# Kernel tuning notes

Hardware: AMD Instinct MI355X
Metric: run time of the kernel (lower is better)

The kernel has to match this reference:

```python
import jax, jax.numpy as jnp
import numpy as np

N_NODES = 100000
N_EDGES = 1600000
IN_CH = 24
OUT_CH = 128


def _linear_params(key, fan_in, fan_out):
    k1, k2 = jax.random.split(key)
    s = 1.0 / np.sqrt(fan_in)
    w = jax.random.uniform(k1, (fan_in, fan_out), jnp.float32, -s, s)
    b = jax.random.uniform(k2, (fan_out,), jnp.float32, -s, s)
    return w, b


def setup_inputs() -> dict:
    key = jax.random.key(0)
    ks = jax.random.split(key, 10)
    x = jax.random.normal(ks[0], (N_NODES, IN_CH), jnp.float32)
    edge_index = jax.random.randint(ks[1], (2, N_EDGES), 0, N_NODES, jnp.int64)
    w1a, b1a = _linear_params(ks[2], 2 * IN_CH, OUT_CH)
    w1b, b1b = _linear_params(ks[3], OUT_CH, OUT_CH)
    w2a, b2a = _linear_params(ks[4], 2 * OUT_CH, OUT_CH)
    w2b, b2b = _linear_params(ks[5], OUT_CH, OUT_CH)
    w3a, b3a = _linear_params(ks[6], 2 * OUT_CH, OUT_CH)
    w3b, b3b = _linear_params(ks[7], OUT_CH, OUT_CH)
    fw, fb = _linear_params(ks[8], 16, 1)
    return dict(x=x, edge_index=edge_index,
                w1a=w1a, b1a=b1a, w1b=w1b, b1b=b1b,
                w2a=w2a, b2a=b2a, w2b=w2b, b2b=b2b,
                w3a=w3a, b3a=b3a, w3b=w3b, b3b=b3b,
                fw=fw, fb=fb)


def _edge_conv(x, src, dst, wa, ba, wb, bb):
    # gather endpoints: x_i = target, x_j = source (PyG convention)
    x_i = x[dst]
    x_j = x[src]
    tmp = jnp.concatenate([x_i, x_j - x_i], axis=1)        # [E, 2*C]
    msg = jax.nn.relu(tmp @ wa + ba) @ wb + bb             # [E, out]
    agg = jax.ops.segment_max(msg, dst, num_segments=N_NODES)
    # PyG max-aggr yields 0 for nodes with no incoming edges
    return jnp.where(jnp.isneginf(agg), 0.0, agg)


def reference(x, edge_index, w1a, b1a, w1b, b1b, w2a, b2a, w2b, b2b,
              w3a, b3a, w3b, b3b, fw, fb):
    src = edge_index[0]
    dst = edge_index[1]
    x2 = jax.nn.relu(_edge_conv(x, src, dst, w1a, b1a, w1b, b1b))
    x4 = jax.nn.relu(_edge_conv(x2, src, dst, w2a, b2a, w2b, b2b))
    x6 = jax.nn.relu(_edge_conv(x4, src, dst, w3a, b3a, w3b, b3b))
    x7 = jnp.concatenate([x2, x4, x6], axis=1)             # [N, 3*OUT_CH]
    # MaxPool1d(kernel=IN_CH, stride=IN_CH) over last dim: 384 -> 16
    x8 = x7.reshape(N_NODES, 3 * OUT_CH // IN_CH, IN_CH).max(axis=-1)
    return x8 @ fw + fb                                     # [N, 1]
```

## Files before the change

### kernel.cpp

```cpp
#include <hip/hip_runtime.h>
#include <stdint.h>

#define NN 100000
#define NE 1600000
#define MAXD 64

using short8 = __attribute__((ext_vector_type(8))) short;
using f32x4  = __attribute__((ext_vector_type(4))) float;
using u32x4  = __attribute__((ext_vector_type(4))) unsigned int;
typedef unsigned short ushort_t;

__device__ __forceinline__ ushort_t f2bf(float f){
  union { float f; uint32_t u; } v; v.f = f;
  uint32_t u = v.u;
  uint32_t r = (u + 0x7fffu + ((u >> 16) & 1u)) >> 16;
  return (ushort_t)r;
}
__device__ __forceinline__ float bf2f(ushort_t h){
  union { uint32_t u; float f; } v; v.u = ((uint32_t)h) << 16;
  return v.f;
}

__global__ void k_detect(const unsigned* ei, int* flag){
  __shared__ int any;
  if(threadIdx.x == 0) any = 0;
  __syncthreads();
  unsigned w = ei[2*threadIdx.x + 1];
  if(w) atomicOr(&any, 1);
  __syncthreads();
  if(threadIdx.x == 0) *flag = (any == 0) ? 1 : 0;
}

__global__ void k_build(const int* ei, const int* flag, int* cursor, int* list){
  int e = blockIdx.x * blockDim.x + threadIdx.x;
  if(e >= NE) return;
  bool i64 = (*flag != 0);
  int src, dst;
  if(i64){
    const long long* p = (const long long*)ei;
    src = (int)p[e]; dst = (int)p[NE + e];
  } else {
    src = ei[e]; dst = ei[NE + e];
  }
  if((unsigned)src >= NN || (unsigned)dst >= NN) return;
  int pos = atomicAdd(&cursor[dst], 1);
  if(pos < MAXD) list[dst*MAXD + pos] = src;
}

__global__ void k_wcatfrag(const float* wa, ushort_t* dst, int C, int KT){
  int idx = blockIdx.x*blockDim.x + threadIdx.x;
  int total = 16*KT*64*8;
  if(idx >= total) return;
  int j = idx & 7, lane = (idx>>3)&63;
  int rest = idx >> 9;
  int kt = rest % KT, nt = rest / KT;
  int k = kt*32 + ((lane>>4)<<3) + j;
  int n = nt*16 + (lane & 15);
  float v = 0.f;
  if(k < C) v = (n < 128) ? (wa[k*128+n] - wa[(C+k)*128+n]) : wa[(C+k)*128 + (n-128)];
  dst[idx] = f2bf(v);
}

__global__ void k_wbfrag(const float* wb, ushort_t* dst){
  int idx = blockIdx.x*blockDim.x + threadIdx.x;
  if(idx >= 8*4*64*8) return;
  int j = idx & 7, lane = (idx>>3)&63;
  int kt = (idx>>9)&3, nt = idx>>11;
  int k = kt*32 + ((lane>>4)<<3) + j;
  int n = nt*16 + (lane & 15);
  dst[idx] = f2bf(wb[k*128 + n]);
}

template<int KT, int ROWLEN, bool SPLIT>
__global__ __launch_bounds__(256)
void k_gemm(const void* xin_, const ushort_t* __restrict__ wfrag,
            const float* __restrict__ bias, float* __restrict__ Atab,
            ushort_t* __restrict__ Btab)
{
  constexpr int K  = KT*32;
  constexpr int RB = K*2 + 16;
  __shared__ ushort_t shHi[64*RB/2];
  __shared__ ushort_t shLo[SPLIT ? 64*RB/2 : 2];

  const int t = threadIdx.x;
  const int wave = t >> 6, lane = t & 63;
  const int l15 = lane & 15, lg = lane >> 4;

  short8 bf[4][KT];
  #pragma unroll
  for(int ntl=0; ntl<4; ntl++)
    #pragma unroll
    for(int kt=0; kt<KT; kt++){
      int nt = wave*4 + ntl;
      bf[ntl][kt] = *(const short8*)&wfrag[((nt*KT + kt)*64 + lane)*8];
    }
  float bv[4] = {0.f,0.f,0.f,0.f};
  if(wave < 2){
    #pragma unroll
    for(int ntl=0; ntl<4; ntl++) bv[ntl] = bias[wave*64 + ntl*16 + l15];
  }

  const int row0 = blockIdx.x * 64;

  constexpr int GROUPS = 64*(K/8);
  #pragma unroll
  for(int it=0; it<GROUPS/256; it++){
    int gi  = t + it*256;
    int row = gi / (K/8), kg = gi % (K/8);
    int gr  = row0 + row;
    int off = (row*RB + kg*16) >> 1;
    if constexpr (SPLIT){
      const float* xin = (const float*)xin_;
      short8 hi8, lo8;
      #pragma unroll
      for(int j=0;j<8;j++){
        int k = kg*8 + j;
        float v = (gr < NN && k < ROWLEN) ? xin[(size_t)gr*ROWLEN + k] : 0.f;
        ushort_t h = f2bf(v);
        hi8[j] = (short)h;
        lo8[j] = (short)f2bf(v - bf2f(h));
      }
      *(short8*)&shHi[off] = hi8;
      *(short8*)&shLo[off] = lo8;
    } else {
      const ushort_t* xb = (const ushort_t*)xin_;
      short8 h8 = {0,0,0,0,0,0,0,0};
      if(gr < NN) h8 = *(const short8*)&xb[(size_t)gr*ROWLEN + kg*8];
      *(short8*)&shHi[off] = h8;
    }
  }
  __syncthreads();

  #pragma unroll
  for(int mc=0; mc<4; mc++){
    f32x4 acc[4];
    #pragma unroll
    for(int ntl=0; ntl<4; ntl++) acc[ntl] = (f32x4){0.f,0.f,0.f,0.f};
    #pragma unroll
    for(int kt=0; kt<KT; kt++){
      int off = ((mc*16 + l15)*RB + kt*64 + lg*16) >> 1;
      short8 ah = *(const short8*)&shHi[off];
      #pragma unroll
      for(int ntl=0; ntl<4; ntl++)
        acc[ntl] = __builtin_amdgcn_mfma_f32_16x16x32_bf16(ah, bf[ntl][kt], acc[ntl], 0,0,0);
      if constexpr (SPLIT){
        short8 al = *(const short8*)&shLo[off];
        #pragma unroll
        for(int ntl=0; ntl<4; ntl++)
          acc[ntl] = __builtin_amdgcn_mfma_f32_16x16x32_bf16(al, bf[ntl][kt], acc[ntl], 0,0,0);
      }
    }
    #pragma unroll
    for(int ntl=0; ntl<4; ntl++){
      #pragma unroll
      for(int q=0; q<4; q++){
        int gr = row0 + mc*16 + lg*4 + q;
        if(gr < NN){
          if(wave < 2){
            int ch = wave*64 + ntl*16 + l15;
            Atab[(size_t)gr*128 + ch] = acc[ntl][q] + bv[ntl];
          } else {
            int ch = (wave-2)*64 + ntl*16 + l15;
            Btab[(size_t)gr*128 + ch] = f2bf(acc[ntl][q]);
          }
        }
      }
    }
  }
}

template<bool F32OUT>
__global__ __launch_bounds__(256)
void k_edge(const float* __restrict__ Atab, const ushort_t* __restrict__ Btab,
            const ushort_t* __restrict__ wbfrag, const float* __restrict__ bias2,
            const int* __restrict__ deg, const int* __restrict__ list,
            float* __restrict__ outF, ushort_t* __restrict__ outB)
{
  __shared__ ushort_t shH[2][16*272/2];

  const int t = threadIdx.x;
  const int wave = t >> 6, lane = t & 63;
  const int l15 = lane & 15, lg = lane >> 4;
  const int eg  = t >> 4;
  const int cg  = t & 15;

  short8 wf[2][4];
  #pragma unroll
  for(int ntl=0; ntl<2; ntl++)
    #pragma unroll
    for(int kt=0; kt<4; kt++){
      int nt = wave*2 + ntl;
      wf[ntl][kt] = *(const short8*)&wbfrag[((nt*4 + kt)*64 + lane)*8];
    }
  float bbv[2];
  #pragma unroll
  for(int ntl=0; ntl<2; ntl++) bbv[ntl] = bias2[wave*32 + ntl*16 + l15];

  int buf = 0;
  for(int n = blockIdx.x; n < NN; n += gridDim.x){
    int d = deg[n]; if(d > MAXD) d = MAXD;
    if(d == 0){
      if(lane < 16){
        #pragma unroll
        for(int ntl=0; ntl<2; ntl++){
          int ch = wave*32 + ntl*16 + lane;
          if(F32OUT) outF[(size_t)n*128 + ch] = 0.f;
          else       outB[(size_t)n*128 + ch] = 0;
        }
      }
      continue;
    }
    const int* lst = &list[(size_t)n*MAXD];
    const float4* ap = (const float4*)&Atab[(size_t)n*128 + cg*8];
    float4 a0 = ap[0], a1 = ap[1];
    float af[8] = {a0.x,a0.y,a0.z,a0.w,a1.x,a1.y,a1.z,a1.w};

    f32x4 mac0 = (f32x4){-3.0e38f,-3.0e38f,-3.0e38f,-3.0e38f};
    f32x4 mac1 = mac0;

    int nch = (d + 15) >> 4;
    int ei0 = (eg < d) ? eg : d - 1;
    short8 b8 = *(const short8*)&Btab[(size_t)lst[ei0]*128 + cg*8];

    for(int c = 0; c < nch; c++){
      union { short8 s; uint32_t u[4]; } bb; bb.s = b8;
      u32x4 pkv;
      #pragma unroll
      for(int p=0; p<4; p++){
        uint32_t w = bb.u[p];
        float flo = __uint_as_float(w << 16);
        float fhi = __uint_as_float(w & 0xffff0000u);
        float hlo = fmaxf(af[2*p]   + flo, 0.f);
        float hhi = fmaxf(af[2*p+1] + fhi, 0.f);
        uint32_t pw;
        asm("v_cvt_pk_bf16_f32 %0, %1, %2" : "=v"(pw) : "v"(hlo), "v"(hhi));
        pkv[p] = pw;
      }
      *(u32x4*)&shH[buf][(eg*272 + cg*16) >> 1] = pkv;

      if(c + 1 < nch){
        int e2 = (c+1)*16 + eg; if(e2 >= d) e2 = d - 1;
        b8 = *(const short8*)&Btab[(size_t)lst[e2]*128 + cg*8];
      }

      __syncthreads();

      f32x4 acc0 = (f32x4){0.f,0.f,0.f,0.f};
      f32x4 acc1 = (f32x4){0.f,0.f,0.f,0.f};
      #pragma unroll
      for(int kt=0; kt<4; kt++){
        short8 a = *(const short8*)&shH[buf][(l15*272 + kt*64 + lg*16) >> 1];
        acc0 = __builtin_amdgcn_mfma_f32_16x16x32_bf16(a, wf[0][kt], acc0, 0,0,0);
        acc1 = __builtin_amdgcn_mfma_f32_16x16x32_bf16(a, wf[1][kt], acc1, 0,0,0);
      }
      #pragma unroll
      for(int q=0; q<4; q++){
        mac0[q] = fmaxf(mac0[q], acc0[q]);
        mac1[q] = fmaxf(mac1[q], acc1[q]);
      }
      buf ^= 1;
    }

    float mm0 = fmaxf(fmaxf(mac0[0],mac0[1]), fmaxf(mac0[2],mac0[3]));
    mm0 = fmaxf(mm0, __shfl_xor(mm0, 16, 64));
    mm0 = fmaxf(mm0, __shfl_xor(mm0, 32, 64));
    float mm1 = fmaxf(fmaxf(mac1[0],mac1[1]), fmaxf(mac1[2],mac1[3]));
    mm1 = fmaxf(mm1, __shfl_xor(mm1, 16, 64));
    mm1 = fmaxf(mm1, __shfl_xor(mm1, 32, 64));

    if(lane < 16){
      float v0 = fmaxf(mm0 + bbv[0], 0.f);
      float v1 = fmaxf(mm1 + bbv[1], 0.f);
      int ch = wave*32 + lane;
      if(F32OUT){
        outF[(size_t)n*128 + ch]      = v0;
        outF[(size_t)n*128 + ch + 16] = v1;
      } else {
        outB[(size_t)n*128 + ch]      = f2bf(v0);
        outB[(size_t)n*128 + ch + 16] = f2bf(v1);
      }
    }
  }
}

template<bool F32IN>
__global__ __launch_bounds__(256)
void k_final(const void* x2_, const void* x4_, const void* x6_,
             const float* __restrict__ fw, const float* __restrict__ fb,
             float* __restrict__ out)
{
  __shared__ float arr[4][384];
  int wave = threadIdx.x >> 6, lane = threadIdx.x & 63;
  int n = blockIdx.x*4 + wave;
  if(n < NN){
    const void* xs[3] = {x2_, x4_, x6_};
    #pragma unroll
    for(int tt=0; tt<3; tt++){
      float a, b;
      if(F32IN){
        const float* p = (const float*)xs[tt] + (size_t)n*128 + lane*2;
        a = p[0]; b = p[1];
      } else {
        const ushort_t* p = (const ushort_t*)xs[tt] + (size_t)n*128 + lane*2;
        a = bf2f(p[0]); b = bf2f(p[1]);
      }
      arr[wave][tt*128 + lane*2]     = a;
      arr[wave][tt*128 + lane*2 + 1] = b;
    }
  }
  __syncthreads();
  if(n < NN && lane < 16){
    float m = -3.0e38f;
    #pragma unroll
    for(int j=0;j<24;j++) m = fmaxf(m, arr[wave][lane*24 + j]);
    float p = m * fw[lane];
    #pragma unroll
    for(int off=1; off<16; off<<=1) p += __shfl_xor(p, off, 64);
    if(lane == 0) out[n] = p + fb[0];
  }
}

extern "C" void kernel_launch(void* const* d_in, const int* in_sizes, int n_in,
                              void* d_out, int out_size, void* d_ws, size_t ws_size,
                              hipStream_t stream)
{
  const float* x   = (const float*)d_in[0];
  const void*  ei  = d_in[1];
  const float* w1a = (const float*)d_in[2];
  const float* b1a = (const float*)d_in[3];
  const float* w1b = (const float*)d_in[4];
  const float* b1b = (const float*)d_in[5];
  const float* w2a = (const float*)d_in[6];
  const float* b2a = (const float*)d_in[7];
  const float* w2b = (const float*)d_in[8];
  const float* b2b = (const float*)d_in[9];
  const float* w3a = (const float*)d_in[10];
  const float* b3a = (const float*)d_in[11];
  const float* w3b = (const float*)d_in[12];
  const float* b3b = (const float*)d_in[13];
  const float* fw  = (const float*)d_in[14];
  const float* fb  = (const float*)d_in[15];

  char* ws = (char*)d_ws;
  size_t off = 0;
  auto alloc = [&](size_t bytes) -> void* {
    void* p = ws + off;
    off = (off + bytes + 255) & ~(size_t)255;
    return p;
  };
  int*      flag   = (int*)alloc(4);
  int*      cursor = (int*)alloc((size_t)NN*4);
  int*      list   = (int*)alloc((size_t)NN*MAXD*4);
  float*    Atab   = (float*)alloc((size_t)NN*128*4);
  ushort_t* Btab   = (ushort_t*)alloc((size_t)NN*128*2);
  ushort_t* wf1    = (ushort_t*)alloc(16*1*64*8*2);
  ushort_t* wf2    = (ushort_t*)alloc(16*4*64*8*2);
  ushort_t* wf3    = (ushort_t*)alloc(16*4*64*8*2);
  ushort_t* wbf1   = (ushort_t*)alloc(8*4*64*8*2);
  ushort_t* wbf2   = (ushort_t*)alloc(8*4*64*8*2);
  ushort_t* wbf3   = (ushort_t*)alloc(8*4*64*8*2);

  size_t fixed = off;
  bool planA = (ws_size >= fixed + 3*(size_t)NN*128*4 + 1024);
  void *x2, *x4, *x6;
  size_t xbytes = planA ? (size_t)NN*128*4 : (size_t)NN*128*2;
  x2 = alloc(xbytes); x4 = alloc(xbytes); x6 = alloc(xbytes);

  hipMemsetAsync(cursor, 0, (size_t)NN*4, stream);
  k_detect<<<1, 128, 0, stream>>>((const unsigned*)ei, flag);
  k_build<<<(NE + 255)/256, 256, 0, stream>>>((const int*)ei, flag, cursor, list);

  k_wcatfrag<<<(16*1*64*8 + 255)/256, 256, 0, stream>>>(w1a, wf1, 24, 1);
  k_wcatfrag<<<(16*4*64*8 + 255)/256, 256, 0, stream>>>(w2a, wf2, 128, 4);
  k_wcatfrag<<<(16*4*64*8 + 255)/256, 256, 0, stream>>>(w3a, wf3, 128, 4);
  k_wbfrag<<<64, 256, 0, stream>>>(w1b, wbf1);
  k_wbfrag<<<64, 256, 0, stream>>>(w2b, wbf2);
  k_wbfrag<<<64, 256, 0, stream>>>(w3b, wbf3);

  const int GT = (NN + 63)/64;
  const int EG = 4096;

  k_gemm<1,24,true><<<GT, 256, 0, stream>>>(x, wf1, b1a, Atab, Btab);
  if(planA){
    k_edge<true><<<EG, 256, 0, stream>>>(Atab, Btab, wbf1, b1b, cursor, list, (float*)x2, nullptr);
    k_gemm<4,128,true><<<GT, 256, 0, stream>>>(x2, wf2, b2a, Atab, Btab);
    k_edge<true><<<EG, 256, 0, stream>>>(Atab, Btab, wbf2, b2b, cursor, list, (float*)x4, nullptr);
    k_gemm<4,128,true><<<GT, 256, 0, stream>>>(x4, wf3, b3a, Atab, Btab);
    k_edge<true><<<EG, 256, 0, stream>>>(Atab, Btab, wbf3, b3b, cursor, list, (float*)x6, nullptr);
    k_final<true><<<(NN + 3)/4, 256, 0, stream>>>(x2, x4, x6, fw, fb, (float*)d_out);
  } else {
    k_edge<false><<<EG, 256, 0, stream>>>(Atab, Btab, wbf1, b1b, cursor, list, nullptr, (ushort_t*)x2);
    k_gemm<4,128,false><<<GT, 256, 0, stream>>>(x2, wf2, b2a, Atab, Btab);
    k_edge<false><<<EG, 256, 0, stream>>>(Atab, Btab, wbf2, b2b, cursor, list, nullptr, (ushort_t*)x4);
    k_gemm<4,128,false><<<GT, 256, 0, stream>>>(x4, wf3, b3a, Atab, Btab);
    k_edge<false><<<EG, 256, 0, stream>>>(Atab, Btab, wbf3, b3b, cursor, list, nullptr, (ushort_t*)x6);
    k_final<false><<<(NN + 3)/4, 256, 0, stream>>>(x2, x4, x6, fw, fb, (float*)d_out);
  }
}
```

Before: 842.0 us.

## Assign one node per wave in edge kernel, dropping block-wide barriers

The edge kernel now processes one destination node per wavefront instead of one per 256-thread block. Each wave gathers its own 16 neighbor rows, writes them to a private swizzled LDS tile, and computes all 8 output column tiles itself with MFMA. This removes the per-chunk __syncthreads and lets the four waves in a block run independently. In exchange, the second-layer weight fragments are reloaded from global memory on every chunk instead of being held in registers, and register pressure rises, with launch bounds set to request 4 blocks per SM.

```diff
diff --git a/kernel.cpp b/kernel.cpp
--- a/kernel.cpp
+++ b/kernel.cpp
@@ -170,114 +170,118 @@
 }
 
 template<bool F32OUT>
-__global__ __launch_bounds__(256)
+__global__ __launch_bounds__(256, 4)
 void k_edge(const float* __restrict__ Atab, const ushort_t* __restrict__ Btab,
             const ushort_t* __restrict__ wbfrag, const float* __restrict__ bias2,
             const int* __restrict__ deg, const int* __restrict__ list,
             float* __restrict__ outF, ushort_t* __restrict__ outB)
 {
-  __shared__ ushort_t shH[2][16*272/2];
+  __shared__ ushort_t sh[4][16*136];
 
   const int t = threadIdx.x;
   const int wave = t >> 6, lane = t & 63;
-  const int l15 = lane & 15, lg = lane >> 4;
-  const int eg  = t >> 4;
-  const int cg  = t & 15;
-
-  short8 wf[2][4];
+  const int r  = lane & 15;
+  const int qq = lane >> 4;
+  const int sw = ((qq ^ (r & 3)) * 8);
+  const int rbase = r * 136;
+  ushort_t* msh = sh[wave];
+
+  float bb[8];
   #pragma unroll
-  for(int ntl=0; ntl<2; ntl++)
-    #pragma unroll
-    for(int kt=0; kt<4; kt++){
-      int nt = wave*2 + ntl;
-      wf[ntl][kt] = *(const short8*)&wbfrag[((nt*4 + kt)*64 + lane)*8];
-    }
-  float bbv[2];
-  #pragma unroll
-  for(int ntl=0; ntl<2; ntl++) bbv[ntl] = bias2[wave*32 + ntl*16 + l15];
-
-  int buf = 0;
-  for(int n = blockIdx.x; n < NN; n += gridDim.x){
+  for(int nt=0; nt<8; nt++) bb[nt] = bias2[nt*16 + r];
+
+  for(int n = blockIdx.x*4 + wave; n < NN; n += gridDim.x*4){
     int d = deg[n]; if(d > MAXD) d = MAXD;
     if(d == 0){
       if(lane < 16){
         #pragma unroll
-        for(int ntl=0; ntl<2; ntl++){
-          int ch = wave*32 + ntl*16 + lane;
-          if(F32OUT) outF[(size_t)n*128 + ch] = 0.f;
-          else       outB[(size_t)n*128 + ch] = 0;
+        for(int nt=0; nt<8; nt++){
+          if(F32OUT) outF[(size_t)n*128 + nt*16 + lane] = 0.f;
+          else       outB[(size_t)n*128 + nt*16 + lane] = 0;
         }
       }
       continue;
     }
     const int* lst = &list[(size_t)n*MAXD];
-    const float4* ap = (const float4*)&Atab[(size_t)n*128 + cg*8];
-    float4 a0 = ap[0], a1 = ap[1];
-    float af[8] = {a0.x,a0.y,a0.z,a0.w,a1.x,a1.y,a1.z,a1.w};
-
-    f32x4 mac0 = (f32x4){-3.0e38f,-3.0e38f,-3.0e38f,-3.0e38f};
-    f32x4 mac1 = mac0;
+
+    float a[4][8];
+    #pragma unroll
+    for(int i=0;i<4;i++){
+      f32x4 lo = *(const f32x4*)&Atab[(size_t)n*128 + i*32 + qq*8];
+      f32x4 hi = *(const f32x4*)&Atab[(size_t)n*128 + i*32 + qq*8 + 4];
+      #pragma unroll
+      for(int j=0;j<4;j++){ a[i][j] = lo[j]; a[i][4+j] = hi[j]; }
+    }
+
+    f32x4 mac[8];
+    #pragma unroll
+    for(int nt=0;nt<8;nt++)
+      mac[nt] = (f32x4){-3.0e38f,-3.0e38f,-3.0e38f,-3.0e38f};
 
     int nch = (d + 15) >> 4;
-    int ei0 = (eg < d) ? eg : d - 1;
-    short8 b8 = *(const short8*)&Btab[(size_t)lst[ei0]*128 + cg*8];
-
-    for(int c = 0; c < nch; c++){
-      union { short8 s; uint32_t u[4]; } bb; bb.s = b8;
-      u32x4 pkv;
-      #pragma unroll
-      for(int p=0; p<4; p++){
-        uint32_t w = bb.u[p];
-        float flo = __uint_as_float(w << 16);
-        float fhi = __uint_as_float(w & 0xffff0000u);
-        float hlo = fmaxf(af[2*p]   + flo, 0.f);
-        float hhi = fmaxf(af[2*p+1] + fhi, 0.f);
-        uint32_t pw;
-        asm("v_cvt_pk_bf16_f32 %0, %1, %2" : "=v"(pw) : "v"(hlo), "v"(hhi));
-        pkv[p] = pw;
-      }
-      *(u32x4*)&shH[buf][(eg*272 + cg*16) >> 1] = pkv;
+    int e0 = r; if(e0 >= d) e0 = d - 1;
+    int s = lst[e0];
+    short8 bw[4];
+    #pragma unroll
+    for(int i=0;i<4;i++)
+      bw[i] = *(const short8*)&Btab[(size_t)s*128 + i*32 + qq*8];
+
+    for(int c = 0; c < nch; ++c){
+      u32x4 pk[4];
+      #pragma unroll
+      for(int i=0;i<4;i++){
+        union { short8 s8; uint32_t u[4]; } ub; ub.s8 = bw[i];
+        #pragma unroll
+        for(int w2=0; w2<4; ++w2){
+          uint32_t u = ub.u[w2];
+          float flo = __uint_as_float(u << 16);
+          float fhi = __uint_as_float(u & 0xffff0000u);
+          float hlo = fmaxf(a[i][2*w2]   + flo, 0.f);
+          float hhi = fmaxf(a[i][2*w2+1] + fhi, 0.f);
+          uint32_t pw;
+          asm("v_cvt_pk_bf16_f32 %0, %1, %2" : "=v"(pw) : "v"(hlo), "v"(hhi));
+          pk[i][w2] = pw;
+        }
+      }
+      asm volatile("s_waitcnt lgkmcnt(0)" ::: "memory");
+      #pragma unroll
+      for(int i=0;i<4;i++)
+        *(u32x4*)&msh[rbase + i*32 + sw] = pk[i];
 
       if(c + 1 < nch){
-        int e2 = (c+1)*16 + eg; if(e2 >= d) e2 = d - 1;
-        b8 = *(const short8*)&Btab[(size_t)lst[e2]*128 + cg*8];
-      }
-
-      __syncthreads();
-
-      f32x4 acc0 = (f32x4){0.f,0.f,0.f,0.f};
-      f32x4 acc1 = (f32x4){0.f,0.f,0.f,0.f};
-      #pragma unroll
-      for(int kt=0; kt<4; kt++){
-        short8 a = *(const short8*)&shH[buf][(l15*272 + kt*64 + lg*16) >> 1];
-        acc0 = __builtin_amdgcn_mfma_f32_16x16x32_bf16(a, wf[0][kt], acc0, 0,0,0);
-        acc1 = __builtin_amdgcn_mfma_f32_16x16x32_bf16(a, wf[1][kt], acc1, 0,0,0);
-      }
-      #pragma unroll
-      for(int q=0; q<4; q++){
-        mac0[q] = fmaxf(mac0[q], acc0[q]);
-        mac1[q] = fmaxf(mac1[q], acc1[q]);
-      }
-      buf ^= 1;
-    }
-
-    float mm0 = fmaxf(fmaxf(mac0[0],mac0[1]), fmaxf(mac0[2],mac0[3]));
-    mm0 = fmaxf(mm0, __shfl_xor(mm0, 16, 64));
-    mm0 = fmaxf(mm0, __shfl_xor(mm0, 32, 64));
-    float mm1 = fmaxf(fmaxf(mac1[0],mac1[1]), fmaxf(mac1[2],mac1[3]));
-    mm1 = fmaxf(mm1, __shfl_xor(mm1, 16, 64));
-    mm1 = fmaxf(mm1, __shfl_xor(mm1, 32, 64));
-
-    if(lane < 16){
-      float v0 = fmaxf(mm0 + bbv[0], 0.f);
-      float v1 = fmaxf(mm1 + bbv[1], 0.f);
-      int ch = wave*32 + lane;
-      if(F32OUT){
-        outF[(size_t)n*128 + ch]      = v0;
-        outF[(size_t)n*128 + ch + 16] = v1;
-      } else {
-        outB[(size_t)n*128 + ch]      = f2bf(v0);
-        outB[(size_t)n*128 + ch + 16] = f2bf(v1);
+        int e2 = (c+1)*16 + r; if(e2 >= d) e2 = d - 1;
+        s = lst[e2];
+        #pragma unroll
+        for(int i=0;i<4;i++)
+          bw[i] = *(const short8*)&Btab[(size_t)s*128 + i*32 + qq*8];
+      }
+
+      short8 af[4];
+      #pragma unroll
+      for(int kt=0; kt<4; ++kt)
+        af[kt] = *(const short8*)&msh[rbase + kt*32 + sw];
+      #pragma unroll
+      for(int nt=0; nt<8; ++nt){
+        f32x4 acc = (f32x4){0.f,0.f,0.f,0.f};
+        #pragma unroll
+        for(int kt=0; kt<4; ++kt){
+          short8 wfr = *(const short8*)&wbfrag[((nt*4 + kt)*64 + lane)*8];
+          acc = __builtin_amdgcn_mfma_f32_16x16x32_bf16(af[kt], wfr, acc, 0,0,0);
+        }
+        #pragma unroll
+        for(int q=0;q<4;q++) mac[nt][q] = fmaxf(mac[nt][q], acc[q]);
+      }
+    }
+
+    #pragma unroll
+    for(int nt=0; nt<8; ++nt){
+      float m = fmaxf(fmaxf(mac[nt][0],mac[nt][1]), fmaxf(mac[nt][2],mac[nt][3]));
+      m = fmaxf(m, __shfl_xor(m, 16, 64));
+      m = fmaxf(m, __shfl_xor(m, 32, 64));
+      float v = fmaxf(m + bb[nt], 0.f);
+      if(lane < 16){
+        if(F32OUT) outF[(size_t)n*128 + nt*16 + lane] = v;
+        else       outB[(size_t)n*128 + nt*16 + lane] = f2bf(v);
       }
     }
   }
```

Measured after the change: 2.544 ms. 202% more time.

## Process two destination nodes per block iteration in edge kernel

Applied to the files above, without the earlier changes.

The edge-message kernel now handles a pair of destination nodes per loop iteration. Each node has its own LDS staging buffers, running max accumulators and gather prefetches, and both share one barrier per chunk. This is meant to halve the number of __syncthreads per node and keep more gather loads and MFMA work in flight to hide memory latency. In exchange it raises register pressure and adds per-node branches, and when the two nodes differ in degree the extra chunks only partly fill the work.

```diff
diff --git a/kernel.cpp b/kernel.cpp
--- a/kernel.cpp
+++ b/kernel.cpp
@@ -176,7 +176,7 @@
             const int* __restrict__ deg, const int* __restrict__ list,
             float* __restrict__ outF, ushort_t* __restrict__ outB)
 {
-  __shared__ ushort_t shH[2][16*272/2];
+  __shared__ ushort_t shH[2][2][16*136];
 
   const int t = threadIdx.x;
   const int wave = t >> 6, lane = t & 63;
@@ -197,87 +197,174 @@
   for(int ntl=0; ntl<2; ntl++) bbv[ntl] = bias2[wave*32 + ntl*16 + l15];
 
   int buf = 0;
-  for(int n = blockIdx.x; n < NN; n += gridDim.x){
-    int d = deg[n]; if(d > MAXD) d = MAXD;
-    if(d == 0){
+  for(int base = blockIdx.x*2; base < NN; base += gridDim.x*2){
+    const int n0 = base, n1 = base + 1;
+    int d0 = deg[n0]; if(d0 > MAXD) d0 = MAXD;
+    int d1 = (n1 < NN) ? deg[n1] : 0; if(d1 > MAXD) d1 = MAXD;
+
+    if(d0 == 0 && lane < 16){
+      #pragma unroll
+      for(int ntl=0; ntl<2; ntl++){
+        int ch = wave*32 + ntl*16 + lane;
+        if(F32OUT) outF[(size_t)n0*128 + ch] = 0.f;
+        else       outB[(size_t)n0*128 + ch] = 0;
+      }
+    }
+    if(n1 < NN && d1 == 0 && lane < 16){
+      #pragma unroll
+      for(int ntl=0; ntl<2; ntl++){
+        int ch = wave*32 + ntl*16 + lane;
+        if(F32OUT) outF[(size_t)n1*128 + ch] = 0.f;
+        else       outB[(size_t)n1*128 + ch] = 0;
+      }
+    }
+
+    const int nch0 = (d0 + 15) >> 4;
+    const int nch1 = (d1 + 15) >> 4;
+    const int ncmax = nch0 > nch1 ? nch0 : nch1;
+    if(ncmax == 0) continue;
+
+    const int* lst0 = &list[(size_t)n0*MAXD];
+    const int* lst1 = &list[(size_t)n1*MAXD];
+
+    float af0[8], af1[8];
+    short8 b80, b81;
+    f32x4 mac00, mac01, mac10, mac11;
+    mac00 = mac01 = mac10 = mac11 = (f32x4){-3.0e38f,-3.0e38f,-3.0e38f,-3.0e38f};
+
+    if(nch0){
+      const float4* ap = (const float4*)&Atab[(size_t)n0*128 + cg*8];
+      float4 a0 = ap[0], a1 = ap[1];
+      af0[0]=a0.x; af0[1]=a0.y; af0[2]=a0.z; af0[3]=a0.w;
+      af0[4]=a1.x; af0[5]=a1.y; af0[6]=a1.z; af0[7]=a1.w;
+      int e0 = (eg < d0) ? eg : d0 - 1;
+      b80 = *(const short8*)&Btab[(size_t)lst0[e0]*128 + cg*8];
+    }
+    if(nch1){
+      const float4* ap = (const float4*)&Atab[(size_t)n1*128 + cg*8];
+      float4 a0 = ap[0], a1 = ap[1];
+      af1[0]=a0.x; af1[1]=a0.y; af1[2]=a0.z; af1[3]=a0.w;
+      af1[4]=a1.x; af1[5]=a1.y; af1[6]=a1.z; af1[7]=a1.w;
+      int e0 = (eg < d1) ? eg : d1 - 1;
+      b81 = *(const short8*)&Btab[(size_t)lst1[e0]*128 + cg*8];
+    }
+
+    for(int c = 0; c < ncmax; ++c){
+      if(c < nch0){
+        union { short8 s8; uint32_t u[4]; } ub; ub.s8 = b80;
+        u32x4 pkv;
+        #pragma unroll
+        for(int p=0; p<4; ++p){
+          uint32_t u = ub.u[p];
+          float flo = __uint_as_float(u << 16);
+          float fhi = __uint_as_float(u & 0xffff0000u);
+          float hlo = fmaxf(af0[2*p]   + flo, 0.f);
+          float hhi = fmaxf(af0[2*p+1] + fhi, 0.f);
+          uint32_t pw;
+          asm("v_cvt_pk_bf16_f32 %0, %1, %2" : "=v"(pw) : "v"(hlo), "v"(hhi));
+          pkv[p] = pw;
+        }
+        *(u32x4*)&shH[0][buf][eg*136 + cg*8] = pkv;
+      }
+      if(c < nch1){
+        union { short8 s8; uint32_t u[4]; } ub; ub.s8 = b81;
+        u32x4 pkv;
+        #pragma unroll
+        for(int p=0; p<4; ++p){
+          uint32_t u = ub.u[p];
+          float flo = __uint_as_float(u << 16);
+          float fhi = __uint_as_float(u & 0xffff0000u);
+          float hlo = fmaxf(af1[2*p]   + flo, 0.f);
+          float hhi = fmaxf(af1[2*p+1] + fhi, 0.f);
+          uint32_t pw;
+          asm("v_cvt_pk_bf16_f32 %0, %1, %2" : "=v"(pw) : "v"(hlo), "v"(hhi));
+          pkv[p] = pw;
+        }
+        *(u32x4*)&shH[1][buf][eg*136 + cg*8] = pkv;
+      }
+
+      if(c + 1 < nch0){
+        int e2 = (c+1)*16 + eg; if(e2 >= d0) e2 = d0 - 1;
+        b80 = *(const short8*)&Btab[(size_t)lst0[e2]*128 + cg*8];
+      }
+      if(c + 1 < nch1){
+        int e2 = (c+1)*16 + eg; if(e2 >= d1) e2 = d1 - 1;
+        b81 = *(const short8*)&Btab[(size_t)lst1[e2]*128 + cg*8];
+      }
+
+      __syncthreads();
+
+      if(c < nch0){
+        f32x4 acc0 = (f32x4){0.f,0.f,0.f,0.f};
+        f32x4 acc1 = (f32x4){0.f,0.f,0.f,0.f};
+        #pragma unroll
+        for(int kt=0; kt<4; kt++){
+          short8 a = *(const short8*)&shH[0][buf][l15*136 + kt*32 + lg*8];
+          acc0 = __builtin_amdgcn_mfma_f32_16x16x32_bf16(a, wf[0][kt], acc0, 0,0,0);
+          acc1 = __builtin_amdgcn_mfma_f32_16x16x32_bf16(a, wf[1][kt], acc1, 0,0,0);
+        }
+        #pragma unroll
+        for(int q=0; q<4; q++){
+          mac00[q] = fmaxf(mac00[q], acc0[q]);
+          mac01[q] = fmaxf(mac01[q], acc1[q]);
+        }
+      }
+      if(c < nch1){
+        f32x4 acc0 = (f32x4){0.f,0.f,0.f,0.f};
+        f32x4 acc1 = (f32x4){0.f,0.f,0.f,0.f};
+        #pragma unroll
+        for(int kt=0; kt<4; kt++){
+          short8 a = *(const short8*)&shH[1][buf][l15*136 + kt*32 + lg*8];
+          acc0 = __builtin_amdgcn_mfma_f32_16x16x32_bf16(a, wf[0][kt], acc0, 0,0,0);
+          acc1 = __builtin_amdgcn_mfma_f32_16x16x32_bf16(a, wf[1][kt], acc1, 0,0,0);
+        }
+        #pragma unroll
+        for(int q=0; q<4; q++){
+          mac10[q] = fmaxf(mac10[q], acc0[q]);
+          mac11[q] = fmaxf(mac11[q], acc1[q]);
+        }
+      }
+      buf ^= 1;
+    }
+
+    if(nch0){
+      float mm0 = fmaxf(fmaxf(mac00[0],mac00[1]), fmaxf(mac00[2],mac00[3]));
+      mm0 = fmaxf(mm0, __shfl_xor(mm0, 16, 64));
+      mm0 = fmaxf(mm0, __shfl_xor(mm0, 32, 64));
+      float mm1 = fmaxf(fmaxf(mac01[0],mac01[1]), fmaxf(mac01[2],mac01[3]));
+      mm1 = fmaxf(mm1, __shfl_xor(mm1, 16, 64));
+      mm1 = fmaxf(mm1, __shfl_xor(mm1, 32, 64));
       if(lane < 16){
-        #pragma unroll
-        for(int ntl=0; ntl<2; ntl++){
-          int ch = wave*32 + ntl*16 + lane;
-          if(F32OUT) outF[(size_t)n*128 + ch] = 0.f;
-          else       outB[(size_t)n*128 + ch] = 0;
-        }
-      }
-      continue;
-    }
-    const int* lst = &list[(size_t)n*MAXD];
-    const float4* ap = (const float4*)&Atab[(size_t)n*128 + cg*8];
-    float4 a0 = ap[0], a1 = ap[1];
-    float af[8] = {a0.x,a0.y,a0.z,a0.w,a1.x,a1.y,a1.z,a1.w};
-
-    f32x4 mac0 = (f32x4){-3.0e38f,-3.0e38f,-3.0e38f,-3.0e38f};
-    f32x4 mac1 = mac0;
-
-    int nch = (d + 15) >> 4;
-    int ei0 = (eg < d) ? eg : d - 1;
-    short8 b8 = *(const short8*)&Btab[(size_t)lst[ei0]*128 + cg*8];
-
-    for(int c = 0; c < nch; c++){
-      union { short8 s; uint32_t u[4]; } bb; bb.s = b8;
-      u32x4 pkv;
-      #pragma unroll
-      for(int p=0; p<4; p++){
-        uint32_t w = bb.u[p];
-        float flo = __uint_as_float(w << 16);
-        float fhi = __uint_as_float(w & 0xffff0000u);
-        float hlo = fmaxf(af[2*p]   + flo, 0.f);
-        float hhi = fmaxf(af[2*p+1] + fhi, 0.f);
-        uint32_t pw;
-        asm("v_cvt_pk_bf16_f32 %0, %1, %2" : "=v"(pw) : "v"(hlo), "v"(hhi));
-        pkv[p] = pw;
-      }
-      *(u32x4*)&shH[buf][(eg*272 + cg*16) >> 1] = pkv;
-
-      if(c + 1 < nch){
-        int e2 = (c+1)*16 + eg; if(e2 >= d) e2 = d - 1;
-        b8 = *(const short8*)&Btab[(size_t)lst[e2]*128 + cg*8];
-      }
-
-      __syncthreads();
-
-      f32x4 acc0 = (f32x4){0.f,0.f,0.f,0.f};
-      f32x4 acc1 = (f32x4){0.f,0.f,0.f,0.f};
-      #pragma unroll
-      for(int kt=0; kt<4; kt++){
-        short8 a = *(const short8*)&shH[buf][(l15*272 + kt*64 + lg*16) >> 1];
-        acc0 = __builtin_amdgcn_mfma_f32_16x16x32_bf16(a, wf[0][kt], acc0, 0,0,0);
-        acc1 = __builtin_amdgcn_mfma_f32_16x16x32_bf16(a, wf[1][kt], acc1, 0,0,0);
-      }
-      #pragma unroll
-      for(int q=0; q<4; q++){
-        mac0[q] = fmaxf(mac0[q], acc0[q]);
-        mac1[q] = fmaxf(mac1[q], acc1[q]);
-      }
-      buf ^= 1;
-    }
-
-    float mm0 = fmaxf(fmaxf(mac0[0],mac0[1]), fmaxf(mac0[2],mac0[3]));
-    mm0 = fmaxf(mm0, __shfl_xor(mm0, 16, 64));
-    mm0 = fmaxf(mm0, __shfl_xor(mm0, 32, 64));
-    float mm1 = fmaxf(fmaxf(mac1[0],mac1[1]), fmaxf(mac1[2],mac1[3]));
-    mm1 = fmaxf(mm1, __shfl_xor(mm1, 16, 64));
-    mm1 = fmaxf(mm1, __shfl_xor(mm1, 32, 64));
-
-    if(lane < 16){
-      float v0 = fmaxf(mm0 + bbv[0], 0.f);
-      float v1 = fmaxf(mm1 + bbv[1], 0.f);
-      int ch = wave*32 + lane;
-      if(F32OUT){
-        outF[(size_t)n*128 + ch]      = v0;
-        outF[(size_t)n*128 + ch + 16] = v1;
-      } else {
-        outB[(size_t)n*128 + ch]      = f2bf(v0);
-        outB[(size_t)n*128 + ch + 16] = f2bf(v1);
+        float v0 = fmaxf(mm0 + bbv[0], 0.f);
+        float v1 = fmaxf(mm1 + bbv[1], 0.f);
+        int ch = wave*32 + lane;
+        if(F32OUT){
+          outF[(size_t)n0*128 + ch]      = v0;
+          outF[(size_t)n0*128 + ch + 16] = v1;
+        } else {
+          outB[(size_t)n0*128 + ch]      = f2bf(v0);
+          outB[(size_t)n0*128 + ch + 16] = f2bf(v1);
+        }
+      }
+    }
+    if(nch1){
+      float mm0 = fmaxf(fmaxf(mac10[0],mac10[1]), fmaxf(mac10[2],mac10[3]));
+      mm0 = fmaxf(mm0, __shfl_xor(mm0, 16, 64));
+      mm0 = fmaxf(mm0, __shfl_xor(mm0, 32, 64));
+      float mm1 = fmaxf(fmaxf(mac11[0],mac11[1]), fmaxf(mac11[2],mac11[3]));
+      mm1 = fmaxf(mm1, __shfl_xor(mm1, 16, 64));
+      mm1 = fmaxf(mm1, __shfl_xor(mm1, 32, 64));
+      if(lane < 16){
+        float v0 = fmaxf(mm0 + bbv[0], 0.f);
+        float v1 = fmaxf(mm1 + bbv[1], 0.f);
+        int ch = wave*32 + lane;
+        if(F32OUT){
+          outF[(size_t)n1*128 + ch]      = v0;
+          outF[(size_t)n1*128 + ch + 16] = v1;
+        } else {
+          outB[(size_t)n1*128 + ch]      = f2bf(v0);
+          outB[(size_t)n1*128 + ch + 16] = f2bf(v1);
+        }
       }
     }
   }
```

After: 863.1 us. 2.5% more time.
